# Optimization experiments

Hardware: AMD Instinct MI355X
Metric: run time of the kernel (lower is better)

Reference implementation:

```python
import jax, jax.numpy as jnp
import numpy as np

N_NODES = 100000
N_EDGES = 3200000
IN_FEATS = 256
OUT_FEATS = 128
N_LAYERS = 3


def setup_inputs() -> dict:
    key = jax.random.key(0)
    k1, k2, k3, k4, k5, k6 = jax.random.split(key, 6)
    x = jax.random.normal(k1, (N_NODES, IN_FEATS), dtype=jnp.float32)
    row = jax.random.randint(k2, (N_EDGES,), 0, N_NODES, dtype=jnp.int64)
    col = jax.random.randint(k3, (N_EDGES,), 0, N_NODES, dtype=jnp.int64)
    vals = jax.random.uniform(k4, (N_EDGES,), dtype=jnp.float32)
    W = jax.random.normal(k5, (OUT_FEATS, IN_FEATS), dtype=jnp.float32) * (1.0 / np.sqrt(IN_FEATS))
    b = jax.random.normal(k6, (OUT_FEATS,), dtype=jnp.float32) * 0.01
    return {"x": x, "row": row, "col": col, "vals": vals, "W": W, "b": b, "n_layers": N_LAYERS}


def reference(x, row, col, vals, W, b, n_layers):
    n_nodes = x.shape[0]
    # z = linear(x)
    z = jnp.einsum('ni,oi->no', x, W) + b  # [N, out_feats]
    # repeated SpMM: z_new[r] = sum over edges e with row[e]==r of vals[e] * z[col[e]]
    for _ in range(int(n_layers)):
        gathered = vals[:, None] * z[col]  # [E, out_feats]
        z = jax.ops.segment_sum(gathered, row, num_segments=n_nodes)
    return z
```

## Files before the change

### kernel.cpp

```cpp
#include <hip/hip_runtime.h>
#include <hip/hip_bf16.h>

#define NNODES   100000
#define INF      256
#define OUTF     128
#define NLAYERS  3

#define RPB   196
#define NBKT  511
#define CAP   7168
#define EPB   8192

typedef unsigned short u16;

typedef __attribute__((ext_vector_type(8))) __bf16 bf16x8;
typedef __attribute__((ext_vector_type(4))) float  f32x4;

__device__ __forceinline__ float bf2f(u16 u) {
    union { unsigned int i; float f; } c; c.i = ((unsigned int)u) << 16; return c.f;
}
__device__ __forceinline__ u16 f2bf(float f) {
    union { float f; unsigned int i; } c; c.f = f;
    unsigned int lsb = (c.i >> 16) & 1;
    return (u16)((c.i + 0x7FFF + lsb) >> 16);
}

__global__ __launch_bounds__(256) void wconv_kernel(const float* __restrict__ W,
                                                    u16* __restrict__ Wbf) {
    int i = (blockIdx.x * 256 + threadIdx.x) * 4;
    float4 a = *(const float4*)(W + i);
    ushort4 o;
    o.x = f2bf(a.x); o.y = f2bf(a.y); o.z = f2bf(a.z); o.w = f2bf(a.w);
    *(ushort4*)(Wbf + i) = o;
}

__global__ __launch_bounds__(256) void partition_kernel(
    const int* __restrict__ row, const int* __restrict__ col,
    const float* __restrict__ vals, int* __restrict__ alloc,
    int2* __restrict__ epart, int E)
{
    __shared__ int hist[NBKT];
    __shared__ int gbase[NBKT];
    int tid = threadIdx.x;
    int e0  = blockIdx.x * EPB;

    for (int i = tid; i < NBKT; i += 256) hist[i] = 0;
    __syncthreads();
    for (int i = tid * 4; i < EPB; i += 1024) {
        int e = e0 + i;
        if (e < E) {
            int4 r4 = *(const int4*)(row + e);
            atomicAdd(&hist[r4.x / RPB], 1);
            atomicAdd(&hist[r4.y / RPB], 1);
            atomicAdd(&hist[r4.z / RPB], 1);
            atomicAdd(&hist[r4.w / RPB], 1);
        }
    }
    __syncthreads();
    for (int i = tid; i < NBKT; i += 256) {
        int c = hist[i];
        gbase[i] = c ? atomicAdd(&alloc[i], c) : 0;
    }
    __syncthreads();
    for (int i = tid; i < NBKT; i += 256) hist[i] = 0;
    __syncthreads();
    for (int i = tid * 4; i < EPB; i += 1024) {
        int e = e0 + i;
        if (e < E) {
            int4   r4 = *(const int4*)(row + e);
            int4   c4 = *(const int4*)(col + e);
            float4 v4 = *(const float4*)(vals + e);
            int   rr[4] = {r4.x, r4.y, r4.z, r4.w};
            int   cc[4] = {c4.x, c4.y, c4.z, c4.w};
            float vv[4] = {v4.x, v4.y, v4.z, v4.w};
#pragma unroll
            for (int t = 0; t < 4; ++t) {
                int b    = rr[t] / RPB;
                int lofs = atomicAdd(&hist[b], 1);
                epart[(size_t)b * CAP + gbase[b] + lofs] =
                    make_int2(cc[t] | ((rr[t] - b * RPB) << 17), __float_as_int(vv[t]));
            }
        }
    }
}

__global__ __launch_bounds__(256) void bucket_scatter_kernel(
    const int* __restrict__ alloc, int2* __restrict__ epart,
    int* __restrict__ rowptr, int* __restrict__ rowcnt, int M)
{
    int b = blockIdx.x;
    int n = alloc[b];
    int2* src = epart + (size_t)b * CAP;
    __shared__ int2 stage[CAP];
    __shared__ int  hist[256];
    __shared__ int  excl[256];
    __shared__ int  wofs[RPB];
    int tid = threadIdx.x;

    for (int i = tid; i < n; i += 256) stage[i] = src[i];
    hist[tid] = 0;
    __syncthreads();
    for (int i = tid; i < n; i += 256) atomicAdd(&hist[stage[i].x >> 17], 1);
    __syncthreads();
    int v = hist[tid];
    int w = (v + 1) & ~1;
    excl[tid] = w;
    __syncthreads();
    for (int off = 1; off < 256; off <<= 1) {
        int t = (tid >= off) ? excl[tid - off] : 0;
        __syncthreads();
        excl[tid] += t;
        __syncthreads();
    }
    int ex = excl[tid] - w;
    int r  = b * RPB + tid;
    if (tid < RPB && r < M) {
        rowptr[r] = b * CAP + ex;
        rowcnt[r] = v;
    }
    if (tid < RPB) wofs[tid] = ex;
    __syncthreads();
    for (int i = tid; i < n; i += 256) {
        int2 p  = stage[i];
        int  rl = p.x >> 17;
        int  pos = atomicAdd(&wofs[rl], 1);
        src[pos] = make_int2(p.x & 0x1FFFF, p.y);
    }
}

__global__ __launch_bounds__(256) void gemm_mfma_kernel(
    const float* __restrict__ x, const u16* __restrict__ Wbf,
    const float* __restrict__ b, u16* __restrict__ z, int M)
{
    __shared__ __align__(16) u16 Wl[128 * 256];
    int tid  = threadIdx.x;
    int lane = tid & 63;
    int wv   = tid >> 6;

    {
        int c = tid >> 1;
        int h = tid & 1;
        const bf16x8* src = (const bf16x8*)(Wbf + c * 256 + h * 128);
        u16* dst = Wl + c * 256;
        int swz = c & 7;
#pragma unroll
        for (int t = 0; t < 16; ++t) {
            int j = h * 16 + t;
            *(bf16x8*)(dst + 8 * (j ^ swz)) = src[t];
        }
    }

    int cl = lane & 15;
    int g  = lane >> 4;
    float bo[8];
#pragma unroll
    for (int f = 0; f < 8; ++f) bo[f] = b[16 * f + cl];

    __syncthreads();

    int n0 = blockIdx.x * 64 + wv * 16;
    int nr = n0 + cl;
    if (nr >= M) nr = M - 1;
    const float* xrow = x + (size_t)nr * INF + 8 * g;

    f32x4 acc[8];
#pragma unroll
    for (int f = 0; f < 8; ++f) {
        f32x4 a; a[0] = bo[f]; a[1] = bo[f]; a[2] = bo[f]; a[3] = bo[f];
        acc[f] = a;
    }

#pragma unroll
    for (int ks = 0; ks < 8; ++ks) {
        int k0 = ks * 32;
        float4 a0 = ((const float4*)(xrow + k0))[0];
        float4 a1 = ((const float4*)(xrow + k0))[1];
        bf16x8 af;
        af[0] = (__bf16)a0.x; af[1] = (__bf16)a0.y;
        af[2] = (__bf16)a0.z; af[3] = (__bf16)a0.w;
        af[4] = (__bf16)a1.x; af[5] = (__bf16)a1.y;
        af[6] = (__bf16)a1.z; af[7] = (__bf16)a1.w;
#pragma unroll
        for (int f = 0; f < 8; ++f) {
            int c  = 16 * f + cl;
            int ke = (k0 + 8 * g) ^ ((c & 7) << 3);
            bf16x8 bfr = *(const bf16x8*)(Wl + c * 256 + ke);
            acc[f] = __builtin_amdgcn_mfma_f32_16x16x32_bf16(af, bfr, acc[f], 0, 0, 0);
        }
    }

    int rbase = n0 + 4 * g;
#pragma unroll
    for (int j = 0; j < 4; ++j) {
        int n = rbase + j;
        if (n < M) {
            u16* zr = z + (size_t)n * OUTF;
#pragma unroll
            for (int f = 0; f < 8; ++f)
                zr[16 * f + cl] = f2bf(acc[f][j]);
        }
    }
}

template <bool MASKED>
__device__ __forceinline__ void edge8(const int2* __restrict__ ep, int e, int end,
                                      const u16* __restrict__ zin, int f,
                                      float2* __restrict__ acc) {
    int2 p[8];
#pragma unroll
    for (int i = 0; i < 8; ++i) {
        int idx = MASKED ? ((e + i < end) ? e + i : end - 1) : (e + i);
        p[i] = ep[idx];
    }
    ushort2 zb[8];
#pragma unroll
    for (int i = 0; i < 8; ++i)
        zb[i] = *(const ushort2*)(zin + (size_t)p[i].x * OUTF + f);
#pragma unroll
    for (int i = 0; i < 8; ++i) {
        float v = __int_as_float(p[i].y);
        if (MASKED) v = (e + i < end) ? v : 0.f;
        acc[i & 3].x += v * bf2f(zb[i].x);
        acc[i & 3].y += v * bf2f(zb[i].y);
    }
}

template <bool OUT_BF16>
__global__ __launch_bounds__(256) void spmm_kernel(const int* __restrict__ rowptr,
                                                   const int* __restrict__ rowcnt,
                                                   const int2* __restrict__ epart,
                                                   const u16* __restrict__ zin,
                                                   void* __restrict__ zout, int M) {
    int r = blockIdx.x * 4 + (threadIdx.x >> 6);
    if (r >= M) return;
    int lane = threadIdx.x & 63;
    int f    = lane * 2;

    int start = __builtin_amdgcn_readfirstlane(rowptr[r]);
    int n     = __builtin_amdgcn_readfirstlane(rowcnt[r]);
    int end   = start + n;

    float2 acc[4] = {{0.f,0.f},{0.f,0.f},{0.f,0.f},{0.f,0.f}};
    int e = start;
    for (; e + 16 <= end; e += 16) {
        int4 q[8];
#pragma unroll
        for (int j = 0; j < 8; ++j) q[j] = *((const int4*)(epart + e) + j);
        __builtin_amdgcn_sched_barrier(0);
        ushort2 zb[16];
#pragma unroll
        for (int j = 0; j < 8; ++j) {
            zb[2*j]   = *(const ushort2*)(zin + (size_t)q[j].x * OUTF + f);
            zb[2*j+1] = *(const ushort2*)(zin + (size_t)q[j].z * OUTF + f);
        }
        __builtin_amdgcn_sched_barrier(0);
#pragma unroll
        for (int j = 0; j < 8; ++j) {
            float v0 = __int_as_float(q[j].y);
            float v1 = __int_as_float(q[j].w);
            acc[(2*j)   & 3].x += v0 * bf2f(zb[2*j].x);
            acc[(2*j)   & 3].y += v0 * bf2f(zb[2*j].y);
            acc[(2*j+1) & 3].x += v1 * bf2f(zb[2*j+1].x);
            acc[(2*j+1) & 3].y += v1 * bf2f(zb[2*j+1].y);
        }
    }
    for (; e < end; e += 8) edge8<true>(epart, e, end, zin, f, acc);

    float sx = (acc[0].x + acc[1].x) + (acc[2].x + acc[3].x);
    float sy = (acc[0].y + acc[1].y) + (acc[2].y + acc[3].y);
    if (OUT_BF16) {
        ushort2 o; o.x = f2bf(sx); o.y = f2bf(sy);
        *(ushort2*)((u16*)zout + (size_t)r * OUTF + f) = o;
    } else {
        *(float2*)((float*)zout + (size_t)r * OUTF + f) = make_float2(sx, sy);
    }
}


extern "C" void kernel_launch(void* const* d_in, const int* in_sizes, int n_in,
                              void* d_out, int out_size, void* d_ws, size_t ws_size,
                              hipStream_t stream) {
    const float* x    = (const float*)d_in[0];
    const int*   row  = (const int*)d_in[1];
    const int*   col  = (const int*)d_in[2];
    const float* vals = (const float*)d_in[3];
    const float* W    = (const float*)d_in[4];
    const float* b    = (const float*)d_in[5];
    float* out = (float*)d_out;

    const int M = in_sizes[0] / INF;
    const int E = in_sizes[1];

    u16*   zb0    = (u16*)d_ws;
    u16*   zb1    = zb0 + (size_t)M * OUTF;
    int*   rowptr = (int*)(zb1 + (size_t)M * OUTF);
    int*   rowcnt = rowptr + M;
    int*   alloc  = rowcnt + M;
    size_t wb_ofs = (size_t)((char*)(alloc + NBKT) - (char*)d_ws);
    wb_ofs = (wb_ofs + 15) & ~(size_t)15;
    u16*   Wbf    = (u16*)((char*)d_ws + wb_ofs);
    size_t ep_ofs = wb_ofs + (size_t)OUTF * INF * sizeof(u16);
    ep_ofs = (ep_ofs + 15) & ~(size_t)15;
    int2*  epart  = (int2*)((char*)d_ws + ep_ofs);

    wconv_kernel<<<(OUTF * INF) / 1024, 256, 0, stream>>>(W, Wbf);

    hipMemsetAsync(alloc, 0, NBKT * sizeof(int), stream);
    partition_kernel<<<(E + EPB - 1) / EPB, 256, 0, stream>>>(row, col, vals, alloc, epart, E);
    bucket_scatter_kernel<<<NBKT, 256, 0, stream>>>(alloc, epart, rowptr, rowcnt, M);

    gemm_mfma_kernel<<<(M + 63) / 64, 256, 0, stream>>>(x, Wbf, b, zb0, M);

    int sgrid = (M + 3) / 4;
    spmm_kernel<true ><<<sgrid, 256, 0, stream>>>(rowptr, rowcnt, epart, zb0, (void*)zb1, M);
    spmm_kernel<true ><<<sgrid, 256, 0, stream>>>(rowptr, rowcnt, epart, zb1, (void*)zb0, M);
    spmm_kernel<false><<<sgrid, 256, 0, stream>>>(rowptr, rowcnt, epart, zb0, (void*)out, M);
}
```

Measured before the change: 608.8 us.

## Replace bucketed two-pass CSR build with global count-scan-scatter

Builds the row-sorted edge list by counting node degrees with global atomics, running a three-kernel prefix scan, and then scattering edges with per-row global atomic cursors. This removes the fixed-capacity bucket partition and the LDS staging pass in favour of a direct CSR build. In exchange it adds more kernel launches and heavy global atomic traffic on 100K counters. Edges within a row land in nondeterministic order and locality is worse than the bucketed writes, which may also change SpMM gather locality.

```diff
diff --git a/kernel.cpp b/kernel.cpp
--- a/kernel.cpp
+++ b/kernel.cpp
@@ -6,10 +6,8 @@
 #define OUTF     128
 #define NLAYERS  3
 
-#define RPB   196
-#define NBKT  511
-#define CAP   7168
-#define EPB   8192
+#define SCAN_BLK 1024
+#define NSB      ((NNODES + SCAN_BLK - 1) / SCAN_BLK)
 
 typedef unsigned short u16;
 
@@ -34,97 +32,110 @@
     *(ushort4*)(Wbf + i) = o;
 }
 
-__global__ __launch_bounds__(256) void partition_kernel(
-    const int* __restrict__ row, const int* __restrict__ col,
-    const float* __restrict__ vals, int* __restrict__ alloc,
-    int2* __restrict__ epart, int E)
-{
-    __shared__ int hist[NBKT];
-    __shared__ int gbase[NBKT];
+
+__global__ __launch_bounds__(256) void count_kernel(const int* __restrict__ row,
+                                                    int* __restrict__ deg, int E)
+{
+    int e = (blockIdx.x * 256 + threadIdx.x) * 4;
+    if (e + 3 < E) {
+        int4 r4 = *(const int4*)(row + e);
+        atomicAdd(&deg[r4.x], 1);
+        atomicAdd(&deg[r4.y], 1);
+        atomicAdd(&deg[r4.z], 1);
+        atomicAdd(&deg[r4.w], 1);
+    } else {
+        for (; e < E; ++e) atomicAdd(&deg[row[e]], 1);
+    }
+}
+
+__global__ __launch_bounds__(256) void scan1_kernel(const int* __restrict__ deg,
+                                                    int* __restrict__ rowptr,
+                                                    int* __restrict__ btot, int M)
+{
+    __shared__ int sc[256];
     int tid = threadIdx.x;
-    int e0  = blockIdx.x * EPB;
-
-    for (int i = tid; i < NBKT; i += 256) hist[i] = 0;
-    __syncthreads();
-    for (int i = tid * 4; i < EPB; i += 1024) {
-        int e = e0 + i;
-        if (e < E) {
-            int4 r4 = *(const int4*)(row + e);
-            atomicAdd(&hist[r4.x / RPB], 1);
-            atomicAdd(&hist[r4.y / RPB], 1);
-            atomicAdd(&hist[r4.z / RPB], 1);
-            atomicAdd(&hist[r4.w / RPB], 1);
-        }
-    }
-    __syncthreads();
-    for (int i = tid; i < NBKT; i += 256) {
-        int c = hist[i];
-        gbase[i] = c ? atomicAdd(&alloc[i], c) : 0;
-    }
-    __syncthreads();
-    for (int i = tid; i < NBKT; i += 256) hist[i] = 0;
-    __syncthreads();
-    for (int i = tid * 4; i < EPB; i += 1024) {
-        int e = e0 + i;
-        if (e < E) {
-            int4   r4 = *(const int4*)(row + e);
-            int4   c4 = *(const int4*)(col + e);
-            float4 v4 = *(const float4*)(vals + e);
-            int   rr[4] = {r4.x, r4.y, r4.z, r4.w};
-            int   cc[4] = {c4.x, c4.y, c4.z, c4.w};
-            float vv[4] = {v4.x, v4.y, v4.z, v4.w};
-#pragma unroll
-            for (int t = 0; t < 4; ++t) {
-                int b    = rr[t] / RPB;
-                int lofs = atomicAdd(&hist[b], 1);
-                epart[(size_t)b * CAP + gbase[b] + lofs] =
-                    make_int2(cc[t] | ((rr[t] - b * RPB) << 17), __float_as_int(vv[t]));
-            }
-        }
-    }
-}
-
-__global__ __launch_bounds__(256) void bucket_scatter_kernel(
-    const int* __restrict__ alloc, int2* __restrict__ epart,
-    int* __restrict__ rowptr, int* __restrict__ rowcnt, int M)
-{
-    int b = blockIdx.x;
-    int n = alloc[b];
-    int2* src = epart + (size_t)b * CAP;
-    __shared__ int2 stage[CAP];
-    __shared__ int  hist[256];
-    __shared__ int  excl[256];
-    __shared__ int  wofs[RPB];
-    int tid = threadIdx.x;
-
-    for (int i = tid; i < n; i += 256) stage[i] = src[i];
-    hist[tid] = 0;
-    __syncthreads();
-    for (int i = tid; i < n; i += 256) atomicAdd(&hist[stage[i].x >> 17], 1);
-    __syncthreads();
-    int v = hist[tid];
-    int w = (v + 1) & ~1;
-    excl[tid] = w;
+    int r0  = blockIdx.x * SCAN_BLK + tid * 4;
+    int w[4]; int s = 0;
+#pragma unroll
+    for (int i = 0; i < 4; ++i) {
+        int r = r0 + i;
+        int d = (r < M) ? deg[r] : 0;
+        w[i] = s;
+        s += (d + 1) & ~1;
+    }
+    sc[tid] = s;
     __syncthreads();
     for (int off = 1; off < 256; off <<= 1) {
-        int t = (tid >= off) ? excl[tid - off] : 0;
+        int t = (tid >= off) ? sc[tid - off] : 0;
         __syncthreads();
-        excl[tid] += t;
+        sc[tid] += t;
         __syncthreads();
     }
-    int ex = excl[tid] - w;
-    int r  = b * RPB + tid;
-    if (tid < RPB && r < M) {
-        rowptr[r] = b * CAP + ex;
-        rowcnt[r] = v;
-    }
-    if (tid < RPB) wofs[tid] = ex;
+    int bex = sc[tid] - s;
+#pragma unroll
+    for (int i = 0; i < 4; ++i) {
+        int r = r0 + i;
+        if (r < M) rowptr[r] = bex + w[i];
+    }
+    if (tid == 0) btot[blockIdx.x] = sc[255];
+}
+
+__global__ __launch_bounds__(128) void scan2_kernel(int* __restrict__ btot)
+{
+    __shared__ int sc[128];
+    int tid = threadIdx.x;
+    int v = (tid < NSB) ? btot[tid] : 0;
+    sc[tid] = v;
     __syncthreads();
-    for (int i = tid; i < n; i += 256) {
-        int2 p  = stage[i];
-        int  rl = p.x >> 17;
-        int  pos = atomicAdd(&wofs[rl], 1);
-        src[pos] = make_int2(p.x & 0x1FFFF, p.y);
+    for (int off = 1; off < 128; off <<= 1) {
+        int t = (tid >= off) ? sc[tid - off] : 0;
+        __syncthreads();
+        sc[tid] += t;
+        __syncthreads();
+    }
+    if (tid < NSB) btot[tid] = sc[tid] - v;
+}
+
+__global__ __launch_bounds__(256) void scan3_kernel(int* __restrict__ rowptr,
+                                                    int* __restrict__ cursor,
+                                                    const int* __restrict__ btot, int M)
+{
+    int base = btot[blockIdx.x];
+    int r0   = blockIdx.x * SCAN_BLK + threadIdx.x * 4;
+#pragma unroll
+    for (int i = 0; i < 4; ++i) {
+        int r = r0 + i;
+        if (r < M) {
+            int p = rowptr[r] + base;
+            rowptr[r] = p;
+            cursor[r] = p;
+        }
+    }
+}
+
+__global__ __launch_bounds__(256) void scatter_kernel(
+    const int* __restrict__ row, const int* __restrict__ col,
+    const float* __restrict__ vals, int* __restrict__ cursor,
+    int2* __restrict__ epart, int E)
+{
+    int e = (blockIdx.x * 256 + threadIdx.x) * 4;
+    if (e + 3 < E) {
+        int4   r4 = *(const int4*)(row + e);
+        int4   c4 = *(const int4*)(col + e);
+        float4 v4 = *(const float4*)(vals + e);
+        int p0 = atomicAdd(&cursor[r4.x], 1);
+        int p1 = atomicAdd(&cursor[r4.y], 1);
+        int p2 = atomicAdd(&cursor[r4.z], 1);
+        int p3 = atomicAdd(&cursor[r4.w], 1);
+        epart[p0] = make_int2(c4.x, __float_as_int(v4.x));
+        epart[p1] = make_int2(c4.y, __float_as_int(v4.y));
+        epart[p2] = make_int2(c4.z, __float_as_int(v4.z));
+        epart[p3] = make_int2(c4.w, __float_as_int(v4.w));
+    } else {
+        for (; e < E; ++e) {
+            int p = atomicAdd(&cursor[row[e]], 1);
+            epart[p] = make_int2(col[e], __float_as_int(vals[e]));
+        }
     }
 }
 
@@ -295,8 +306,9 @@
     u16*   zb1    = zb0 + (size_t)M * OUTF;
     int*   rowptr = (int*)(zb1 + (size_t)M * OUTF);
     int*   rowcnt = rowptr + M;
-    int*   alloc  = rowcnt + M;
-    size_t wb_ofs = (size_t)((char*)(alloc + NBKT) - (char*)d_ws);
+    int*   cursor = rowcnt + M;
+    int*   btot   = cursor + M;
+    size_t wb_ofs = (size_t)((char*)(btot + NSB) - (char*)d_ws);
     wb_ofs = (wb_ofs + 15) & ~(size_t)15;
     u16*   Wbf    = (u16*)((char*)d_ws + wb_ofs);
     size_t ep_ofs = wb_ofs + (size_t)OUTF * INF * sizeof(u16);
@@ -305,9 +317,13 @@
 
     wconv_kernel<<<(OUTF * INF) / 1024, 256, 0, stream>>>(W, Wbf);
 
-    hipMemsetAsync(alloc, 0, NBKT * sizeof(int), stream);
-    partition_kernel<<<(E + EPB - 1) / EPB, 256, 0, stream>>>(row, col, vals, alloc, epart, E);
-    bucket_scatter_kernel<<<NBKT, 256, 0, stream>>>(alloc, epart, rowptr, rowcnt, M);
+    hipMemsetAsync(rowcnt, 0, (size_t)M * sizeof(int), stream);
+    int egrid = (E + 1023) / 1024;
+    count_kernel<<<egrid, 256, 0, stream>>>(row, rowcnt, E);
+    scan1_kernel<<<NSB, 256, 0, stream>>>(rowcnt, rowptr, btot, M);
+    scan2_kernel<<<1, 128, 0, stream>>>(btot);
+    scan3_kernel<<<NSB, 256, 0, stream>>>(rowptr, cursor, btot, M);
+    scatter_kernel<<<egrid, 256, 0, stream>>>(row, col, vals, cursor, epart, E);
 
     gemm_mfma_kernel<<<(M + 63) / 64, 256, 0, stream>>>(x, Wbf, b, zb0, M);
 
```

Measured after the change: 911.9 us. +49.8%, slower.
